# Optimization experiments

Hardware: AMD Instinct MI355X
Metric: run time of the kernel (lower is better)

The kernel has to match this reference:

```python
import jax, jax.numpy as jnp
import numpy as np

B, S, D, H, DQ, DV = 4, 1024, 1024, 16, 64, 64
EPS = 1e-5  # torch LayerNorm default


def setup_inputs() -> dict:
    key = jax.random.key(0)
    ks = jax.random.split(key, 6)
    x = jax.random.normal(ks[0], (B, S, D), dtype=jnp.float32)
    scale = 0.02
    return {
        "query_sequences": x,
        "key_sequences": x,   # self-attention: identical tensors
        "value_sequences": x,
        "key_value_sequence_lengths": jax.random.randint(ks[1], (B,), 512, S + 1, dtype=jnp.int32),
        "ln_gamma": jnp.ones((D,), jnp.float32),
        "ln_beta": jnp.zeros((D,), jnp.float32),
        "Wq": scale * jax.random.normal(ks[2], (D, H * DQ), jnp.float32),
        "bq": jnp.zeros((H * DQ,), jnp.float32),
        "Wk": scale * jax.random.normal(ks[3], (D, H * DQ), jnp.float32),
        "bk": jnp.zeros((H * DQ,), jnp.float32),
        "Wv": scale * jax.random.normal(ks[4], (D, H * DV), jnp.float32),
        "bv": jnp.zeros((H * DV,), jnp.float32),
    }


def _layer_norm(x, gamma, beta):
    mu = jnp.mean(x, axis=-1, keepdims=True)
    var = jnp.mean(jnp.square(x - mu), axis=-1, keepdims=True)
    return (x - mu) * jax.lax.rsqrt(var + EPS) * gamma + beta


def reference(query_sequences, key_sequences, value_sequences,
              key_value_sequence_lengths, ln_gamma, ln_beta,
              Wq, bq, Wk, bk, Wv, bv):
    # self-attention path (query/key/value sequences are identical):
    # pre-LayerNorm applied to all three, causal + pad masking, dropout=0.
    x_in = query_sequences
    xn = _layer_norm(x_in, ln_gamma, ln_beta)

    q = (xn @ Wq + bq).reshape(B, S, H, DQ).transpose(0, 2, 1, 3)  # (B,H,S,DQ)
    k = (xn @ Wk + bk).reshape(B, S, H, DQ).transpose(0, 2, 1, 3)
    v = (xn @ Wv + bv).reshape(B, S, H, DV).transpose(0, 2, 1, 3)

    scores = jnp.einsum("bhqd,bhkd->bhqk", q, k) * (1.0 / np.sqrt(DQ))

    kv_pos = jnp.arange(S)
    pad_mask = kv_pos[None, None, None, :] < key_value_sequence_lengths[:, None, None, None]
    causal = jnp.tril(jnp.ones((S, S), dtype=bool))[None, None]
    mask = pad_mask & causal
    scores = jnp.where(mask, scores, -jnp.inf)

    attn = jax.nn.softmax(scores, axis=-1)  # (B,H,S,S)

    out = jnp.einsum("bhqk,bhkd->bhqd", attn, v)          # (B,H,S,DV)
    out = out.transpose(0, 2, 1, 3).reshape(B, S, H * DV)  # (B,S,D)
    # d_model == n_heads*d_values -> cast_output is Identity; residual is plain sum
    seq = x_in + out
    return seq, attn
```

## Files before the change

kernel.cpp:

```cpp
#include <hip/hip_runtime.h>
#include <stdint.h>

#define BB 4
#define SS 1024
#define DD 1024
#define HH 16

typedef __attribute__((ext_vector_type(8))) __bf16 bf16x8;
typedef __attribute__((ext_vector_type(4))) float f32x4;

__device__ __forceinline__ unsigned short f2bf(float f) {
  union { float ff; uint32_t u; } a; a.ff = f;
  uint32_t r = a.u + 0x7fffu + ((a.u >> 16) & 1u);
  return (unsigned short)(r >> 16);
}

__device__ __forceinline__ float bf2f(unsigned short u) {
  union { uint32_t uu; float ff; } a; a.uu = ((uint32_t)u) << 16;
  return a.ff;
}

__device__ __forceinline__ f32x4 mfma16(bf16x8 a, bf16x8 b, f32x4 c) {
  return __builtin_amdgcn_mfma_f32_16x16x32_bf16(a, b, c, 0, 0, 0);
}

__device__ __forceinline__ void async16(const unsigned short* g, unsigned short* l) {
  __builtin_amdgcn_global_load_lds(
      (__attribute__((address_space(1))) void*)(g),
      (__attribute__((address_space(3))) void*)(l), 16u, 0, 0u);
}

__device__ __forceinline__ void nt_store4(float* p, f32x4 v) {
  __builtin_nontemporal_store(v, (f32x4*)p);
}

__global__ __launch_bounds__(256) void wtrans_kernel(const float* __restrict__ Wq,
                                                     const float* __restrict__ Wk,
                                                     const float* __restrict__ Wv,
                                                     unsigned short* __restrict__ Wtq,
                                                     unsigned short* __restrict__ Wtk,
                                                     unsigned short* __restrict__ Wtv) {
  __shared__ unsigned short t[64][65];
  const int z = blockIdx.z;
  const float* W = (z == 0) ? Wq : (z == 1) ? Wk : Wv;
  unsigned short* Wt = (z == 0) ? Wtq : (z == 1) ? Wtk : Wtv;
  const int k0 = blockIdx.x * 64, n0 = blockIdx.y * 64;
  const int c = threadIdx.x & 63, r0 = threadIdx.x >> 6;
#pragma unroll
  for (int i = 0; i < 16; ++i) {
    int r = i * 4 + r0;
    t[r][c] = f2bf(W[(size_t)(k0 + r) * DD + n0 + c]);
  }
  __syncthreads();
#pragma unroll
  for (int i = 0; i < 16; ++i) {
    int n = i * 4 + r0;
    Wt[(size_t)(n0 + n) * DD + k0 + c] = t[c][n];
  }
}

__global__ __launch_bounds__(256) void ln_kernel(const float* __restrict__ X,
                                                 const float* __restrict__ gamma,
                                                 const float* __restrict__ beta,
                                                 unsigned short* __restrict__ Xn) {
  const int row = blockIdx.x;
  const int tid = threadIdx.x;
  const float* xr = X + (size_t)row * DD;
  float4 v = ((const float4*)xr)[tid];
  float s = v.x + v.y + v.z + v.w;
  float s2 = v.x * v.x + v.y * v.y + v.z * v.z + v.w * v.w;
#pragma unroll
  for (int off = 1; off < 64; off <<= 1) {
    s += __shfl_xor(s, off);
    s2 += __shfl_xor(s2, off);
  }
  __shared__ float red[8];
  const int wv = tid >> 6, lane = tid & 63;
  if (lane == 0) { red[wv] = s; red[4 + wv] = s2; }
  __syncthreads();
  s = red[0] + red[1] + red[2] + red[3];
  s2 = red[4] + red[5] + red[6] + red[7];
  const float mu = s * (1.0f / DD);
  const float rs = rsqrtf(s2 * (1.0f / DD) - mu * mu + 1e-5f);
  float4 g = ((const float4*)gamma)[tid];
  float4 bt = ((const float4*)beta)[tid];
  ushort4 o;
  o.x = f2bf((v.x - mu) * rs * g.x + bt.x);
  o.y = f2bf((v.y - mu) * rs * g.y + bt.y);
  o.z = f2bf((v.z - mu) * rs * g.z + bt.z);
  o.w = f2bf((v.w - mu) * rs * g.w + bt.w);
  ((ushort4*)(Xn + (size_t)row * DD))[tid] = o;
}

__global__ __launch_bounds__(256) void gemm_qkv_kernel(
    const unsigned short* __restrict__ Xn,
    const unsigned short* __restrict__ Wtq, const unsigned short* __restrict__ Wtk,
    const unsigned short* __restrict__ Wtv,
    const float* __restrict__ bq, const float* __restrict__ bk, const float* __restrict__ bv,
    unsigned short* __restrict__ Qb, unsigned short* __restrict__ Kb,
    unsigned short* __restrict__ Vt) {
  __shared__ __align__(16) unsigned short smem[128 * 136];
  unsigned short* sA = smem;
  unsigned short* sB = smem + 128 * 32;
  const int z = blockIdx.z;
  const unsigned short* Wt = (z == 0) ? Wtq : (z == 1) ? Wtk : Wtv;
  const float* bias = (z == 0) ? bq : (z == 1) ? bk : bv;
  const int tid = threadIdx.x;
  const int lane = tid & 63, wv = tid >> 6;
  const int quad = lane >> 4, l16 = lane & 15;
  const int m0 = blockIdx.x * 128, n0 = blockIdx.y * 128;
  const int wm = (wv & 1) * 64, wn = (wv >> 1) * 64;

  f32x4 acc[4][4];
#pragma unroll
  for (int i = 0; i < 4; ++i)
#pragma unroll
    for (int j = 0; j < 4; ++j) acc[i][j] = (f32x4){0.f, 0.f, 0.f, 0.f};

  for (int kt = 0; kt < DD; kt += 32) {
    __syncthreads();
#pragma unroll
    for (int it = 0; it < 2; ++it) {
      const int c = it * 256 + tid;
      const int row = c >> 2, kc = c & 3;
      async16(Xn + (size_t)(m0 + row) * DD + kt + kc * 8, &sA[(it * 256 + wv * 64) * 8]);
      async16(Wt + (size_t)(n0 + row) * DD + kt + kc * 8, &sB[(it * 256 + wv * 64) * 8]);
    }
    __syncthreads();
    bf16x8 af[4], bfr[4];
#pragma unroll
    for (int i = 0; i < 4; ++i) af[i] = *(const bf16x8*)&sA[(wm + i * 16 + l16) * 32 + quad * 8];
#pragma unroll
    for (int j = 0; j < 4; ++j) bfr[j] = *(const bf16x8*)&sB[(wn + j * 16 + l16) * 32 + quad * 8];
#pragma unroll
    for (int i = 0; i < 4; ++i)
#pragma unroll
      for (int j = 0; j < 4; ++j) acc[i][j] = mfma16(af[i], bfr[j], acc[i][j]);
  }

  __syncthreads();
  if (z < 2) {
    unsigned short* sC = smem;
#pragma unroll
    for (int i = 0; i < 4; ++i) {
      const int lr0 = wm + i * 16 + quad * 4;
#pragma unroll
      for (int j = 0; j < 4; ++j) {
        const int lc = wn + j * 16 + l16;
        const float bb = bias[n0 + lc];
#pragma unroll
        for (int r = 0; r < 4; ++r) sC[(lr0 + r) * 136 + lc] = f2bf(acc[i][j][r] + bb);
      }
    }
    __syncthreads();
    unsigned short* Out = (z == 0) ? Qb : Kb;
    const int rr = tid >> 4, c8 = (tid & 15) * 8;
#pragma unroll
    for (int it = 0; it < 8; ++it) {
      const int row = it * 16 + rr;
      *(uint4*)&Out[(size_t)(m0 + row) * DD + n0 + c8] = *(const uint4*)&sC[row * 136 + c8];
    }
  } else {
    unsigned short* sC = smem;
#pragma unroll
    for (int i = 0; i < 4; ++i) {
      const int lr0 = wm + i * 16 + quad * 4;
#pragma unroll
      for (int j = 0; j < 4; ++j) {
        const int lc = wn + j * 16 + l16;
        const float bb = bias[n0 + lc];
#pragma unroll
        for (int r = 0; r < 4; ++r) sC[lc * 136 + lr0 + r] = f2bf(acc[i][j][r] + bb);
      }
    }
    __syncthreads();
    const int b = m0 >> 10, s0 = m0 & 1023;
    const int rr = tid >> 4, c8 = (tid & 15) * 8;
#pragma unroll
    for (int it = 0; it < 8; ++it) {
      const int row = it * 16 + rr;
      const int n = n0 + row;
      unsigned short* dst =
          &Vt[((size_t)((b * HH + (n >> 6)) * 64 + (n & 63))) * SS + s0 + c8];
      *(uint4*)dst = *(const uint4*)&sC[row * 136 + c8];
    }
  }
}

__global__ __launch_bounds__(256) void attn_kernel(
    const unsigned short* __restrict__ Qb, const unsigned short* __restrict__ Kb,
    const unsigned short* __restrict__ Vt, const float* __restrict__ X,
    const int* __restrict__ lens, float* __restrict__ seq_out,
    float* __restrict__ attn_out) {
  __shared__ unsigned short sQV[128 * 64];
  __shared__ unsigned short sK[128 * 64];
  __shared__ unsigned short sP[4 * 32 * 128];

  const int tid = threadIdx.x;
  const int lane = tid & 63, wv = tid >> 6;
  const int quad = lane >> 4, l16 = lane & 15;
  const int h = blockIdx.y, b = blockIdx.z;
  const int qt = (b & 2) ? (7 - (int)blockIdx.x) : (int)blockIdx.x;
  const int q0 = qt * 128;
  const int len = lens[b];
  const int KE = min(q0 + 128, len);
  const int NKT = (KE + 127) >> 7;
  const float SCL = 0.1803368801111204f;
  const int s7 = l16 & 7;

#pragma unroll
  for (int it = 0; it < 4; ++it) {
    const int c = it * 256 + tid;
    const int row = c >> 3, ch = (c & 7) ^ (row & 7);
    async16(Qb + (size_t)(b * SS + q0 + row) * DD + h * 64 + ch * 8,
            &sQV[(it * 256 + wv * 64) * 8]);
  }
  __syncthreads();

  bf16x8 qf[2][2];
#pragma unroll
  for (int i = 0; i < 2; ++i)
#pragma unroll
    for (int dd = 0; dd < 2; ++dd)
      qf[i][dd] = *(const bf16x8*)
          &sQV[(wv * 32 + i * 16 + l16) * 64 + ((dd * 4 + quad) ^ s7) * 8];

  float lsum[2][4];
#pragma unroll
  for (int i = 0; i < 2; ++i)
#pragma unroll
    for (int r = 0; r < 4; ++r) lsum[i][r] = 0.f;

  for (int kt = 0; kt < NKT; ++kt) {
    const int k0 = kt * 128;
    __syncthreads();
#pragma unroll
    for (int it = 0; it < 4; ++it) {
      const int c = it * 256 + tid;
      const int row = c >> 3, ch = (c & 7) ^ (row & 7);
      async16(Kb + (size_t)(b * SS + k0 + row) * DD + h * 64 + ch * 8,
              &sK[(it * 256 + wv * 64) * 8]);
    }
    __syncthreads();
    const bool edge = (kt == qt) || (k0 + 128 > len);
#pragma unroll
    for (int j = 0; j < 8; ++j) {
      const bf16x8 kf0 = *(const bf16x8*)&sK[(j * 16 + l16) * 64 + ((0 + quad) ^ s7) * 8];
      const bf16x8 kf1 = *(const bf16x8*)&sK[(j * 16 + l16) * 64 + ((4 + quad) ^ s7) * 8];
      const int k = k0 + j * 16 + l16;
#pragma unroll
      for (int i = 0; i < 2; ++i) {
        f32x4 sc = (f32x4){0.f, 0.f, 0.f, 0.f};
        sc = mfma16(qf[i][0], kf0, sc);
        sc = mfma16(qf[i][1], kf1, sc);
        const int qq = q0 + wv * 32 + i * 16 + quad * 4;
#pragma unroll
        for (int r = 0; r < 4; ++r) {
          float sv = sc[r] * SCL;
          if (edge && ((k > qq + r) || (k >= len))) sv = -1e30f;
          lsum[i][r] += __builtin_amdgcn_exp2f(sv);
        }
      }
    }
  }

  float linv[2][4];
#pragma unroll
  for (int i = 0; i < 2; ++i)
#pragma unroll
    for (int r = 0; r < 4; ++r) {
      float l = lsum[i][r];
      l += __shfl_xor(l, 1);
      l += __shfl_xor(l, 2);
      l += __shfl_xor(l, 4);
      l += __shfl_xor(l, 8);
      linv[i][r] = 1.0f / l;
    }

  f32x4 oacc[2][4];
#pragma unroll
  for (int i = 0; i < 2; ++i)
#pragma unroll
    for (int jv = 0; jv < 4; ++jv) oacc[i][jv] = (f32x4){0.f, 0.f, 0.f, 0.f};

  const size_t abase = (size_t)(b * HH + h) * SS * SS;

  for (int kt = 0; kt < NKT; ++kt) {
    const int k0 = kt * 128;
    __syncthreads();
#pragma unroll
    for (int it = 0; it < 4; ++it) {
      const int c = it * 256 + tid;
      const int krow = c >> 3, kch = (c & 7) ^ (krow & 7);
      async16(Kb + (size_t)(b * SS + k0 + krow) * DD + h * 64 + kch * 8,
              &sK[(it * 256 + wv * 64) * 8]);
      const int vrow = c >> 4, vch = (c & 15) ^ (vrow & 15);
      async16(Vt + ((size_t)((b * HH + h) * 64 + vrow)) * SS + k0 + vch * 8,
              &sQV[(it * 256 + wv * 64) * 8]);
    }
    __syncthreads();
    const bool edge = (kt == qt) || (k0 + 128 > len);
#pragma unroll
    for (int j = 0; j < 8; ++j) {
      const bf16x8 kf0 = *(const bf16x8*)&sK[(j * 16 + l16) * 64 + ((0 + quad) ^ s7) * 8];
      const bf16x8 kf1 = *(const bf16x8*)&sK[(j * 16 + l16) * 64 + ((4 + quad) ^ s7) * 8];
      const int k = k0 + j * 16 + l16;
#pragma unroll
      for (int i = 0; i < 2; ++i) {
        f32x4 sc = (f32x4){0.f, 0.f, 0.f, 0.f};
        sc = mfma16(qf[i][0], kf0, sc);
        sc = mfma16(qf[i][1], kf1, sc);
        const int qq = q0 + wv * 32 + i * 16 + quad * 4;
#pragma unroll
        for (int r = 0; r < 4; ++r) {
          float sv = sc[r] * SCL;
          if (edge && ((k > qq + r) || (k >= len))) sv = -1e30f;
          const float p = __builtin_amdgcn_exp2f(sv) * linv[i][r];
          const int prow = i * 16 + quad * 4 + r;
          const int pch = (2 * j + (l16 >> 3)) ^ (prow & 15);
          sP[wv * 4096 + prow * 128 + pch * 8 + (l16 & 7)] = f2bf(p);
        }
      }
    }
    {
      const int r2 = lane >> 5, c32 = lane & 31;
#pragma unroll
      for (int rr = 0; rr < 32; rr += 2) {
        const int row = rr + r2;
        const int ch = (c32 >> 1) ^ (row & 15);
        ushort4 u = *(const ushort4*)&sP[wv * 4096 + row * 128 + ch * 8 + (c32 & 1) * 4];
        f32x4 f;
        f[0] = bf2f(u.x); f[1] = bf2f(u.y); f[2] = bf2f(u.z); f[3] = bf2f(u.w);
        nt_store4(&attn_out[abase + (size_t)(q0 + wv * 32 + row) * SS + k0 + c32 * 4], f);
      }
    }
#pragma unroll
    for (int kk = 0; kk < 4; ++kk) {
      bf16x8 vf[4];
#pragma unroll
      for (int jv = 0; jv < 4; ++jv)
        vf[jv] = *(const bf16x8*)
            &sQV[(jv * 16 + l16) * 128 + (((kk * 4 + quad) ^ l16) & 15) * 8];
#pragma unroll
      for (int i = 0; i < 2; ++i) {
        const bf16x8 pf = *(const bf16x8*)
            &sP[wv * 4096 + (i * 16 + l16) * 128 + ((kk * 4 + quad) ^ l16) * 8];
#pragma unroll
        for (int jv = 0; jv < 4; ++jv) oacc[i][jv] = mfma16(pf, vf[jv], oacc[i][jv]);
      }
    }
  }

  const int Z = SS - NKT * 128;
  if (Z > 0) {
    const int rr0 = tid >> 3;
    const int cf = (tid & 7) * 4;
    const f32x4 zz = (f32x4){0.f, 0.f, 0.f, 0.f};
    for (int rr = rr0; rr < 128; rr += 32) {
      float* dst = attn_out + abase + (size_t)(q0 + rr) * SS + NKT * 128 + cf;
      for (int c8 = 0; c8 < (Z >> 5); ++c8) nt_store4(dst + c8 * 32, zz);
    }
  }

  __syncthreads();
  {
    float* sPf = (float*)&sP[wv * 4096];
#pragma unroll
    for (int i = 0; i < 2; ++i)
#pragma unroll
      for (int jv = 0; jv < 4; ++jv)
#pragma unroll
        for (int r = 0; r < 4; ++r)
          sPf[(i * 16 + quad * 4 + r) * 64 + jv * 16 + l16] = oacc[i][jv][r];
    const int rr = lane >> 4, c4 = (lane & 15) * 4;
#pragma unroll
    for (int it = 0; it < 8; ++it) {
      const int lrow = it * 4 + rr;
      const size_t idx = (size_t)(b * SS + q0 + wv * 32 + lrow) * DD + h * 64 + c4;
      float4 o = *(const float4*)&sPf[lrow * 64 + c4];
      float4 x = *(const float4*)&X[idx];
      o.x += x.x; o.y += x.y; o.z += x.z; o.w += x.w;
      *(float4*)&seq_out[idx] = o;
    }
  }
}

extern "C" void kernel_launch(void* const* d_in, const int* in_sizes, int n_in,
                              void* d_out, int out_size, void* d_ws, size_t ws_size,
                              hipStream_t stream) {
  (void)in_sizes; (void)n_in; (void)out_size; (void)ws_size;
  const float* X     = (const float*)d_in[0];
  const int*   lens  = (const int*)d_in[3];
  const float* gamma = (const float*)d_in[4];
  const float* beta  = (const float*)d_in[5];
  const float* Wq    = (const float*)d_in[6];
  const float* bq    = (const float*)d_in[7];
  const float* Wk    = (const float*)d_in[8];
  const float* bk    = (const float*)d_in[9];
  const float* Wv    = (const float*)d_in[10];
  const float* bv    = (const float*)d_in[11];

  char* ws = (char*)d_ws;
  unsigned short* Xn  = (unsigned short*)(ws);
  unsigned short* Qb  = (unsigned short*)(ws + ((size_t)8  << 20));
  unsigned short* Kb  = (unsigned short*)(ws + ((size_t)16 << 20));
  unsigned short* Vt  = (unsigned short*)(ws + ((size_t)24 << 20));
  unsigned short* Wtq = (unsigned short*)(ws + ((size_t)32 << 20));
  unsigned short* Wtk = (unsigned short*)(ws + ((size_t)34 << 20));
  unsigned short* Wtv = (unsigned short*)(ws + ((size_t)36 << 20));

  float* seq_out  = (float*)d_out;
  float* attn_out = seq_out + (size_t)BB * SS * DD;

  wtrans_kernel<<<dim3(16, 16, 3), 256, 0, stream>>>(Wq, Wk, Wv, Wtq, Wtk, Wtv);
  ln_kernel<<<dim3(BB * SS), 256, 0, stream>>>(X, gamma, beta, Xn);
  gemm_qkv_kernel<<<dim3(32, 8, 3), 256, 0, stream>>>(Xn, Wtq, Wtk, Wtv, bq, bk, bv, Qb, Kb, Vt);
  attn_kernel<<<dim3(8, HH, BB), 256, 0, stream>>>(Qb, Kb, Vt, X, lens, seq_out, attn_out);
}
```

Before: 416.4 us.

## Keep probabilities in registers via transposed QK MFMA, drop LDS staging of P

Swaps the MFMA operand order so each lane holds four consecutive key columns for one query row. Probabilities are then written to attn_out straight from registers and packed into bf16 A-fragments for the PV MFMA with v_cvt_pk_bf16_f32, so the sP LDS buffer and its write/readback round trip go away. V fragments are gathered in two 8-byte halves so they match the new k ordering. The aim is to cut LDS traffic and shared-memory footprint, and the row-sum reduction needs fewer shuffles. In exchange the global stores become 16-byte per-lane scatters across rows rather than contiguous row segments, and the attention output keeps fp32 precision instead of being rounded through bf16.

```diff
diff --git a/kernel.cpp b/kernel.cpp
--- a/kernel.cpp
+++ b/kernel.cpp
@@ -7,6 +7,7 @@
 #define HH 16
 
 typedef __attribute__((ext_vector_type(8))) __bf16 bf16x8;
+typedef __attribute__((ext_vector_type(4))) __bf16 bf16x4;
 typedef __attribute__((ext_vector_type(4))) float f32x4;
 
 __device__ __forceinline__ unsigned short f2bf(float f) {
@@ -22,6 +23,12 @@
 
 __device__ __forceinline__ f32x4 mfma16(bf16x8 a, bf16x8 b, f32x4 c) {
   return __builtin_amdgcn_mfma_f32_16x16x32_bf16(a, b, c, 0, 0, 0);
+}
+
+__device__ __forceinline__ uint32_t cvtpk(float a, float b) {
+  uint32_t r;
+  asm("v_cvt_pk_bf16_f32 %0, %1, %2" : "=v"(r) : "v"(a), "v"(b));
+  return r;
 }
 
 __device__ __forceinline__ void async16(const unsigned short* g, unsigned short* l) {
@@ -192,9 +199,9 @@
     const unsigned short* __restrict__ Vt, const float* __restrict__ X,
     const int* __restrict__ lens, float* __restrict__ seq_out,
     float* __restrict__ attn_out) {
-  __shared__ unsigned short sQV[128 * 64];
-  __shared__ unsigned short sK[128 * 64];
-  __shared__ unsigned short sP[4 * 32 * 128];
+  __shared__ __align__(16) unsigned short smem[2 * 128 * 64];
+  unsigned short* sQV = smem;
+  unsigned short* sK = smem + 128 * 64;
 
   const int tid = threadIdx.x;
   const int lane = tid & 63, wv = tid >> 6;
@@ -225,11 +232,7 @@
       qf[i][dd] = *(const bf16x8*)
           &sQV[(wv * 32 + i * 16 + l16) * 64 + ((dd * 4 + quad) ^ s7) * 8];
 
-  float lsum[2][4];
-#pragma unroll
-  for (int i = 0; i < 2; ++i)
-#pragma unroll
-    for (int r = 0; r < 4; ++r) lsum[i][r] = 0.f;
+  float lsum[2] = {0.f, 0.f};
 
   for (int kt = 0; kt < NKT; ++kt) {
     const int k0 = kt * 128;
@@ -247,43 +250,41 @@
     for (int j = 0; j < 8; ++j) {
       const bf16x8 kf0 = *(const bf16x8*)&sK[(j * 16 + l16) * 64 + ((0 + quad) ^ s7) * 8];
       const bf16x8 kf1 = *(const bf16x8*)&sK[(j * 16 + l16) * 64 + ((4 + quad) ^ s7) * 8];
-      const int k = k0 + j * 16 + l16;
+      const int kb = k0 + j * 16 + quad * 4;
 #pragma unroll
       for (int i = 0; i < 2; ++i) {
         f32x4 sc = (f32x4){0.f, 0.f, 0.f, 0.f};
-        sc = mfma16(qf[i][0], kf0, sc);
-        sc = mfma16(qf[i][1], kf1, sc);
-        const int qq = q0 + wv * 32 + i * 16 + quad * 4;
+        sc = mfma16(kf0, qf[i][0], sc);
+        sc = mfma16(kf1, qf[i][1], sc);
+        const int qq = q0 + wv * 32 + i * 16 + l16;
 #pragma unroll
         for (int r = 0; r < 4; ++r) {
           float sv = sc[r] * SCL;
-          if (edge && ((k > qq + r) || (k >= len))) sv = -1e30f;
-          lsum[i][r] += __builtin_amdgcn_exp2f(sv);
+          if (edge && ((kb + r > qq) || (kb + r >= len))) sv = -1e30f;
+          lsum[i] += __builtin_amdgcn_exp2f(sv);
         }
       }
     }
   }
 
-  float linv[2][4];
+  float linv[2];
+#pragma unroll
+  for (int i = 0; i < 2; ++i) {
+    float l = lsum[i];
+    l += __shfl_xor(l, 16);
+    l += __shfl_xor(l, 32);
+    linv[i] = 1.0f / l;
+  }
+
+  f32x4 oacc[2][4];
 #pragma unroll
   for (int i = 0; i < 2; ++i)
 #pragma unroll
-    for (int r = 0; r < 4; ++r) {
-      float l = lsum[i][r];
-      l += __shfl_xor(l, 1);
-      l += __shfl_xor(l, 2);
-      l += __shfl_xor(l, 4);
-      l += __shfl_xor(l, 8);
-      linv[i][r] = 1.0f / l;
-    }
-
-  f32x4 oacc[2][4];
-#pragma unroll
-  for (int i = 0; i < 2; ++i)
-#pragma unroll
     for (int jv = 0; jv < 4; ++jv) oacc[i][jv] = (f32x4){0.f, 0.f, 0.f, 0.f};
 
   const size_t abase = (size_t)(b * HH + h) * SS * SS;
+  float* const arowA = attn_out + abase + (size_t)(q0 + wv * 32 + l16) * SS;
+  float* const arowB = arowA + (size_t)16 * SS;
 
   for (int kt = 0; kt < NKT; ++kt) {
     const int k0 = kt * 128;
@@ -300,53 +301,52 @@
     }
     __syncthreads();
     const bool edge = (kt == qt) || (k0 + 128 > len);
+
+    uint32_t afw[2][4][4];
 #pragma unroll
     for (int j = 0; j < 8; ++j) {
       const bf16x8 kf0 = *(const bf16x8*)&sK[(j * 16 + l16) * 64 + ((0 + quad) ^ s7) * 8];
       const bf16x8 kf1 = *(const bf16x8*)&sK[(j * 16 + l16) * 64 + ((4 + quad) ^ s7) * 8];
-      const int k = k0 + j * 16 + l16;
+      const int kb = k0 + j * 16 + quad * 4;
 #pragma unroll
       for (int i = 0; i < 2; ++i) {
         f32x4 sc = (f32x4){0.f, 0.f, 0.f, 0.f};
-        sc = mfma16(qf[i][0], kf0, sc);
-        sc = mfma16(qf[i][1], kf1, sc);
-        const int qq = q0 + wv * 32 + i * 16 + quad * 4;
+        sc = mfma16(kf0, qf[i][0], sc);
+        sc = mfma16(kf1, qf[i][1], sc);
+        const int qq = q0 + wv * 32 + i * 16 + l16;
+        f32x4 p;
 #pragma unroll
         for (int r = 0; r < 4; ++r) {
           float sv = sc[r] * SCL;
-          if (edge && ((k > qq + r) || (k >= len))) sv = -1e30f;
-          const float p = __builtin_amdgcn_exp2f(sv) * linv[i][r];
-          const int prow = i * 16 + quad * 4 + r;
-          const int pch = (2 * j + (l16 >> 3)) ^ (prow & 15);
-          sP[wv * 4096 + prow * 128 + pch * 8 + (l16 & 7)] = f2bf(p);
+          if (edge && ((kb + r > qq) || (kb + r >= len))) sv = -1e30f;
+          p[r] = __builtin_amdgcn_exp2f(sv) * linv[i];
         }
-      }
-    }
-    {
-      const int r2 = lane >> 5, c32 = lane & 31;
-#pragma unroll
-      for (int rr = 0; rr < 32; rr += 2) {
-        const int row = rr + r2;
-        const int ch = (c32 >> 1) ^ (row & 15);
-        ushort4 u = *(const ushort4*)&sP[wv * 4096 + row * 128 + ch * 8 + (c32 & 1) * 4];
-        f32x4 f;
-        f[0] = bf2f(u.x); f[1] = bf2f(u.y); f[2] = bf2f(u.z); f[3] = bf2f(u.w);
-        nt_store4(&attn_out[abase + (size_t)(q0 + wv * 32 + row) * SS + k0 + c32 * 4], f);
-      }
-    }
+        nt_store4((i == 0 ? arowA : arowB) + kb, p);
+        afw[i][j >> 1][(j & 1) * 2 + 0] = cvtpk(p[0], p[1]);
+        afw[i][j >> 1][(j & 1) * 2 + 1] = cvtpk(p[2], p[3]);
+      }
+    }
+
 #pragma unroll
     for (int kk = 0; kk < 4; ++kk) {
-      bf16x8 vf[4];
-#pragma unroll
-      for (int jv = 0; jv < 4; ++jv)
-        vf[jv] = *(const bf16x8*)
-            &sQV[(jv * 16 + l16) * 128 + (((kk * 4 + quad) ^ l16) & 15) * 8];
+      union { bf16x8 v8; bf16x4 v4[2]; } vfu[4];
+      const int g1 = kk * 4 + (quad >> 1);
+      const int boff = (quad & 1) * 8;
+#pragma unroll
+      for (int jv = 0; jv < 4; ++jv) {
+        const char* rowp = (const char*)(sQV + (jv * 16 + l16) * 128);
+        vfu[jv].v4[0] = *(const bf16x4*)(rowp + ((g1 ^ l16) * 16 + boff));
+        vfu[jv].v4[1] = *(const bf16x4*)(rowp + (((g1 + 2) ^ l16) * 16 + boff));
+      }
 #pragma unroll
       for (int i = 0; i < 2; ++i) {
-        const bf16x8 pf = *(const bf16x8*)
-            &sP[wv * 4096 + (i * 16 + l16) * 128 + ((kk * 4 + quad) ^ l16) * 8];
-#pragma unroll
-        for (int jv = 0; jv < 4; ++jv) oacc[i][jv] = mfma16(pf, vf[jv], oacc[i][jv]);
+        union { uint32_t w[4]; bf16x8 v8; } pu;
+        pu.w[0] = afw[i][kk][0];
+        pu.w[1] = afw[i][kk][1];
+        pu.w[2] = afw[i][kk][2];
+        pu.w[3] = afw[i][kk][3];
+#pragma unroll
+        for (int jv = 0; jv < 4; ++jv) oacc[i][jv] = mfma16(pu.v8, vfu[jv].v8, oacc[i][jv]);
       }
     }
   }
@@ -364,7 +364,7 @@
 
   __syncthreads();
   {
-    float* sPf = (float*)&sP[wv * 4096];
+    float* sPf = (float*)smem + wv * 2048;
 #pragma unroll
     for (int i = 0; i < 2; ++i)
 #pragma unroll
```

Result: no change. 419.9 us (+0.8%).
